# Kernel tuning notes

Hardware: AMD Instinct MI355X
Metric: run time of the kernel (lower is better)

Reference implementation:

```python
import jax, jax.numpy as jnp
import numpy as np

MARGIN = 0.3  # init kwarg, mode='norm'


def _pairwise_dist(X):
    # squared euclidean distances, then safe sqrt (matches euc_dist(X.t()).sqrt())
    sq = jnp.sum(X * X, axis=1)                      # [n]
    d2 = sq[:, None] + sq[None, :] - 2.0 * (X @ X.T)  # [n, n]
    d2 = jnp.maximum(d2, 0.0)
    # safe sqrt: avoid inf derivative at 0 (diagonal); forward value identical
    return jnp.where(d2 > 0.0, jnp.sqrt(jnp.where(d2 > 0.0, d2, 1.0)), 0.0)


def setup_inputs() -> dict:
    key = jax.random.key(0)
    kx, ky = jax.random.split(key)
    X = jax.random.normal(kx, (4096, 2048), dtype=jnp.float32)
    Y = jax.random.randint(ky, (4096,), 0, 128, dtype=jnp.int64)
    return {"X": X, "Y": Y}


def reference(X, Y):
    dist = _pairwise_dist(X)                         # [n, n]
    mask = Y[:, None] == Y[None, :]                  # same-identity mask [n, n]
    inf = jnp.array(jnp.inf, dtype=dist.dtype)
    # hardest positive per anchor: max over same-label entries
    dist_ap = jnp.max(jnp.where(mask, dist, -inf), axis=1)  # [n]
    # hardest negative per anchor: min over different-label entries
    dist_an = jnp.min(jnp.where(mask, inf, dist), axis=1)   # [n]
    # mode == 'norm': mean hinge
    return jnp.mean(jnp.maximum(dist_ap - dist_an + MARGIN, 0.0))
```

## Files before the change

kernel.cpp:

```cpp
#include <hip/hip_runtime.h>
#include <hip/hip_bf16.h>
#include <hip/hip_fp8.h>

typedef __attribute__((ext_vector_type(4))) int i32x4;
typedef __attribute__((ext_vector_type(8))) int i32x8;
typedef __attribute__((ext_vector_type(16))) float f32x16;

#define MARGIN 0.3f
#define BIGF 3.0e38f

__device__ __forceinline__ f32x16 mx_mfma(i32x8 a, i32x8 b, f32x16 c) {
    return __builtin_amdgcn_mfma_scale_f32_32x32x64_f8f6f4(
        a, b, c, 0 , 0 ,
        0, 127 , 0, 127 );
}

__device__ __forceinline__ i32x8 ld32(const unsigned char* p) {
    i32x4 lo = *(const i32x4*)p;
    i32x4 hi = *(const i32x4*)(p + 16);
    return __builtin_shufflevector(lo, hi, 0, 1, 2, 3, 4, 5, 6, 7);
}

__global__ __launch_bounds__(256) void convert_norm_kernel(
    const float* __restrict__ X, unsigned char* __restrict__ Xf,
    float* __restrict__ nrm, unsigned* __restrict__ ap,
    unsigned* __restrict__ an, unsigned* __restrict__ cnt, int K) {
    const int wave = threadIdx.x >> 6, lane = threadIdx.x & 63;
    const int row = blockIdx.x * 4 + wave;
    const float* xr = X + (size_t)row * K;
    const size_t pbase = ((size_t)(row >> 5)) << 16;
    const int rsub = row & 31;
    float s = 0.0f;
    for (int c = lane * 8; c < K; c += 64 * 8) {
        float4 v0 = *(const float4*)(xr + c);
        float4 v1 = *(const float4*)(xr + c + 4);
        float f[8] = {v0.x, v0.y, v0.z, v0.w, v1.x, v1.y, v1.z, v1.w};
        union { unsigned char b[8]; uint2 u; } p;
#pragma unroll
        for (int i = 0; i < 8; i++) {
            __hip_fp8_e4m3 q(f[i]);
            p.b[i] = q.__x;
            float d = (float)q;
            s += d * d;
        }
        const int lslot = rsub + (((c >> 5) & 1) << 5);
        unsigned char* dst = Xf + pbase + ((size_t)(c >> 6) << 11)
                             + (lslot << 5) + (c & 31);
        *(uint2*)dst = p.u;
    }
    for (int off = 32; off > 0; off >>= 1) s += __shfl_xor(s, off, 64);
    if (lane == 0) {
        nrm[row] = s;
        ap[row] = 0u;
        an[row] = 0x7F800000u;
        if (row == 0) *cnt = 0u;
    }
}

__global__ __launch_bounds__(256, 4) void gemm_reduce_kernel(
    const unsigned char* __restrict__ Xf, const float* __restrict__ nrm,
    const int* __restrict__ Y, unsigned* __restrict__ ap,
    unsigned* __restrict__ an, unsigned* __restrict__ cnt,
    float* __restrict__ out, int N, int K) {
    __shared__ int sYr[128], sYc[128];
    __shared__ float sNr[128], sNc[128];
    __shared__ float redmax[4][64], redmin[4][64];
    __shared__ float cmax[4][64], cmin[4][64];
    __shared__ float lsum[4];
    __shared__ unsigned s_done;

    const int tid = threadIdx.x;
    const int wave = tid >> 6;
    const int lane = tid & 63;
    const int m = lane & 31;
    const int h = lane >> 5;
    const int wr = wave >> 1;
    const int wc = wave & 1;

    const int NB = N >> 7;
    const int ntri = NB * (NB + 1) / 2;
    const int FULLB = ntri - 16;
    const int nt = K >> 6;

    if ((int)blockIdx.x < FULLB) {
        int bi = blockIdx.x, ti = 0;
        while (bi >= NB - ti) { bi -= NB - ti; ti++; }
        const int tj = ti + bi;
        const int rowBase = ti << 7;
        const int colBase = tj << 7;

        if (tid < 128) {
            sYr[tid] = Y[rowBase + tid];
            sNr[tid] = nrm[rowBase + tid];
        } else {
            const int t0 = tid - 128;
            sYc[t0] = Y[colBase + t0];
            sNc[t0] = nrm[colBase + t0];
        }

        f32x16 acc[2][2];
#pragma unroll
        for (int si = 0; si < 2; si++)
#pragma unroll
            for (int sj = 0; sj < 2; sj++)
#pragma unroll
                for (int rr = 0; rr < 16; rr++) acc[si][sj][rr] = 0.0f;

        const unsigned char* pa[2];
        const unsigned char* pb[2];
#pragma unroll
        for (int si = 0; si < 2; si++)
            pa[si] = Xf + (((size_t)(rowBase >> 5) + wr * 2 + si) << 16) + lane * 32;
#pragma unroll
        for (int sj = 0; sj < 2; sj++)
            pb[sj] = Xf + (((size_t)(colBase >> 5) + wc * 2 + sj) << 16) + lane * 32;

#pragma unroll 4
        for (int t = 0; t < nt; t++) {
            const size_t off = (size_t)t << 11;
            i32x8 a0 = ld32(pa[0] + off);
            i32x8 a1 = ld32(pa[1] + off);
            i32x8 b0 = ld32(pb[0] + off);
            i32x8 b1 = ld32(pb[1] + off);
            acc[0][0] = mx_mfma(a0, b0, acc[0][0]);
            acc[0][1] = mx_mfma(a0, b1, acc[0][1]);
            acc[1][0] = mx_mfma(a1, b0, acc[1][0]);
            acc[1][1] = mx_mfma(a1, b1, acc[1][1]);
        }

        __syncthreads();

        float cdp[2] = {-1.0f, -1.0f};
        float cdn[2] = {BIGF, BIGF};
#pragma unroll
        for (int si = 0; si < 2; si++)
#pragma unroll
            for (int reg = 0; reg < 16; reg++) {
                const int row64 = si * 32 + (reg & 3) + 8 * (reg >> 2) + 4 * h;
                const int rIdx = wr * 64 + row64;
                const int yr = sYr[rIdx];
                const float nr = sNr[rIdx];
                float dp = -1.0f, dn = BIGF;
#pragma unroll
                for (int sj = 0; sj < 2; sj++) {
                    const int cIdx = wc * 64 + sj * 32 + m;
                    float d2 = nr + sNc[cIdx] - 2.0f * acc[si][sj][reg];
                    float d = sqrtf(fmaxf(d2, 0.0f));
                    bool same = (yr == sYc[cIdx]);
                    float vp = same ? d : -1.0f;
                    float vn = same ? BIGF : d;
                    dp = fmaxf(dp, vp);
                    dn = fminf(dn, vn);
                    cdp[sj] = fmaxf(cdp[sj], vp);
                    cdn[sj] = fminf(cdn[sj], vn);
                }
                for (int off = 1; off < 32; off <<= 1) {
                    dp = fmaxf(dp, __shfl_xor(dp, off, 64));
                    dn = fminf(dn, __shfl_xor(dn, off, 64));
                }
                if (m == 0) {
                    redmax[wave][row64] = dp;
                    redmin[wave][row64] = dn;
                }
            }
#pragma unroll
        for (int sj = 0; sj < 2; sj++) {
            cdp[sj] = fmaxf(cdp[sj], __shfl_xor(cdp[sj], 32, 64));
            cdn[sj] = fminf(cdn[sj], __shfl_xor(cdn[sj], 32, 64));
            if (h == 0) {
                cmax[wave][sj * 32 + m] = cdp[sj];
                cmin[wave][sj * 32 + m] = cdn[sj];
            }
        }
        __syncthreads();

        if (tid < 128) {
            const int wr2 = tid >> 6, r64 = tid & 63;
            float mx = fmaxf(redmax[wr2 * 2][r64], redmax[wr2 * 2 + 1][r64]);
            float mn = fminf(redmin[wr2 * 2][r64], redmin[wr2 * 2 + 1][r64]);
            atomicMax(&ap[rowBase + tid], __float_as_uint(fmaxf(mx, 0.0f)));
            atomicMin(&an[rowBase + tid], __float_as_uint(mn));
        } else {
            const int t0 = tid - 128;
            const int wc2 = t0 >> 6, c64 = t0 & 63;
            float mx = fmaxf(cmax[wc2][c64], cmax[2 + wc2][c64]);
            float mn = fminf(cmin[wc2][c64], cmin[2 + wc2][c64]);
            atomicMax(&ap[colBase + t0], __float_as_uint(fmaxf(mx, 0.0f)));
            atomicMin(&an[colBase + t0], __float_as_uint(mn));
        }
    } else {
        const int qid = blockIdx.x - FULLB;
        int bi = FULLB + (qid >> 2), ti = 0;
        while (bi >= NB - ti) { bi -= NB - ti; ti++; }
        const int tj = ti + bi;
        const int q = qid & 3;
        const int rowBase = (ti << 7) + ((q >> 1) << 6);
        const int colBase = (tj << 7) + ((q & 1) << 6);

        f32x16 acc;
#pragma unroll
        for (int rr = 0; rr < 16; rr++) acc[rr] = 0.0f;

        const unsigned char* pa =
            Xf + (((size_t)(rowBase >> 5) + wr) << 16) + lane * 32;
        const unsigned char* pb =
            Xf + (((size_t)(colBase >> 5) + wc) << 16) + lane * 32;

#pragma unroll 4
        for (int t = 0; t < nt; t++) {
            const size_t off = (size_t)t << 11;
            i32x8 a = ld32(pa + off);
            i32x8 b = ld32(pb + off);
            acc = mx_mfma(a, b, acc);
        }

        const int gc = colBase + wc * 32 + m;
        const int yc = Y[gc];
        const float nc = nrm[gc];
        float cdp = -1.0f, cdn = BIGF;
#pragma unroll
        for (int reg = 0; reg < 16; reg++) {
            const int row32 = (reg & 3) + 8 * (reg >> 2) + 4 * h;
            const int gr = rowBase + wr * 32 + row32;
            const int yr = Y[gr];
            const float nr = nrm[gr];
            float d2 = nr + nc - 2.0f * acc[reg];
            float d = sqrtf(fmaxf(d2, 0.0f));
            bool same = (yr == yc);
            float vp = same ? d : -1.0f;
            float vn = same ? BIGF : d;
            cdp = fmaxf(cdp, vp);
            cdn = fminf(cdn, vn);
            float dp = vp, dn = vn;
            for (int off = 1; off < 32; off <<= 1) {
                dp = fmaxf(dp, __shfl_xor(dp, off, 64));
                dn = fminf(dn, __shfl_xor(dn, off, 64));
            }
            if (m == 0) {
                atomicMax(&ap[gr], __float_as_uint(fmaxf(dp, 0.0f)));
                atomicMin(&an[gr], __float_as_uint(dn));
            }
        }
        cdp = fmaxf(cdp, __shfl_xor(cdp, 32, 64));
        cdn = fminf(cdn, __shfl_xor(cdn, 32, 64));
        if (h == 0) {
            atomicMax(&ap[gc], __float_as_uint(fmaxf(cdp, 0.0f)));
            atomicMin(&an[gc], __float_as_uint(cdn));
        }
    }

    __syncthreads();
    if (tid == 0) {
        __threadfence();
        s_done = atomicAdd(cnt, 1u);
    }
    __syncthreads();
    if (s_done == gridDim.x - 1) {
        __threadfence();
        float s = 0.0f;
        for (int i = tid; i < N; i += 256) {
            unsigned ua = __hip_atomic_load(&ap[i], __ATOMIC_RELAXED,
                                            __HIP_MEMORY_SCOPE_AGENT);
            unsigned ub = __hip_atomic_load(&an[i], __ATOMIC_RELAXED,
                                            __HIP_MEMORY_SCOPE_AGENT);
            s += fmaxf(__uint_as_float(ua) - __uint_as_float(ub) + MARGIN, 0.0f);
        }
        for (int off = 32; off > 0; off >>= 1) s += __shfl_xor(s, off, 64);
        if (lane == 0) lsum[wave] = s;
        __syncthreads();
        if (tid == 0)
            out[0] = (lsum[0] + lsum[1] + lsum[2] + lsum[3]) / (float)N;
    }
}

extern "C" void kernel_launch(void* const* d_in, const int* in_sizes, int n_in,
                              void* d_out, int out_size, void* d_ws, size_t ws_size,
                              hipStream_t stream) {
    const float* X = (const float*)d_in[0];
    const int* Y = (const int*)d_in[1];
    float* out = (float*)d_out;
    const int N = in_sizes[1];
    const int K = in_sizes[0] / N;

    char* ws = (char*)d_ws;
    unsigned char* Xf = (unsigned char*)ws;
    float* nrm = (float*)(ws + (size_t)N * K);
    unsigned* ap = (unsigned*)((char*)nrm + (size_t)N * 4);
    unsigned* an = (unsigned*)((char*)ap + (size_t)N * 4);
    unsigned* cnt = (unsigned*)((char*)an + (size_t)N * 4);

    convert_norm_kernel<<<N / 4, 256, 0, stream>>>(X, Xf, nrm, ap, an, cnt, K);
    const int NB = N / 128;
    const int ntri = NB * (NB + 1) / 2;
    const int grid = (ntri - 16) + 64;
    gemm_reduce_kernel<<<grid, 256, 0, stream>>>(Xf, nrm, Y, ap, an, cnt,
                                                 out, N, K);
}
```

Before: 132.2 us.

## Fuse fp8 conversion into GEMM kernel with per-panel ready flags

Merges the fp32-to-fp8 conversion and norm pass into the GEMM-reduce kernel. The first N/32 blocks each convert a 32-row panel and publish a release flag, and GEMM tiles spin-wait on the flags of the panels they need. This removes one kernel launch and the boundary between the two stages so conversion can overlap GEMM work. In exchange it adds a memset launch, spin-wait cost, and lowers occupancy to 3 blocks per CU. It also relies on the producer blocks being scheduled before or alongside the waiting blocks to avoid deadlock.

```diff
diff --git a/kernel.cpp b/kernel.cpp
--- a/kernel.cpp
+++ b/kernel.cpp
@@ -21,46 +21,18 @@
     return __builtin_shufflevector(lo, hi, 0, 1, 2, 3, 4, 5, 6, 7);
 }
 
-__global__ __launch_bounds__(256) void convert_norm_kernel(
+__device__ __forceinline__ void waitpan(const unsigned* f, int n) {
+    for (int i = 0; i < n; i++)
+        while (__hip_atomic_load(&f[i], __ATOMIC_RELAXED,
+                                 __HIP_MEMORY_SCOPE_AGENT) == 0u)
+            __builtin_amdgcn_s_sleep(2);
+}
+
+__global__ __launch_bounds__(256, 3) void fused_kernel(
     const float* __restrict__ X, unsigned char* __restrict__ Xf,
-    float* __restrict__ nrm, unsigned* __restrict__ ap,
-    unsigned* __restrict__ an, unsigned* __restrict__ cnt, int K) {
-    const int wave = threadIdx.x >> 6, lane = threadIdx.x & 63;
-    const int row = blockIdx.x * 4 + wave;
-    const float* xr = X + (size_t)row * K;
-    const size_t pbase = ((size_t)(row >> 5)) << 16;
-    const int rsub = row & 31;
-    float s = 0.0f;
-    for (int c = lane * 8; c < K; c += 64 * 8) {
-        float4 v0 = *(const float4*)(xr + c);
-        float4 v1 = *(const float4*)(xr + c + 4);
-        float f[8] = {v0.x, v0.y, v0.z, v0.w, v1.x, v1.y, v1.z, v1.w};
-        union { unsigned char b[8]; uint2 u; } p;
-#pragma unroll
-        for (int i = 0; i < 8; i++) {
-            __hip_fp8_e4m3 q(f[i]);
-            p.b[i] = q.__x;
-            float d = (float)q;
-            s += d * d;
-        }
-        const int lslot = rsub + (((c >> 5) & 1) << 5);
-        unsigned char* dst = Xf + pbase + ((size_t)(c >> 6) << 11)
-                             + (lslot << 5) + (c & 31);
-        *(uint2*)dst = p.u;
-    }
-    for (int off = 32; off > 0; off >>= 1) s += __shfl_xor(s, off, 64);
-    if (lane == 0) {
-        nrm[row] = s;
-        ap[row] = 0u;
-        an[row] = 0x7F800000u;
-        if (row == 0) *cnt = 0u;
-    }
-}
-
-__global__ __launch_bounds__(256, 4) void gemm_reduce_kernel(
-    const unsigned char* __restrict__ Xf, const float* __restrict__ nrm,
-    const int* __restrict__ Y, unsigned* __restrict__ ap,
-    unsigned* __restrict__ an, unsigned* __restrict__ cnt,
+    float* __restrict__ nrm, const int* __restrict__ Y,
+    unsigned* __restrict__ ap, unsigned* __restrict__ an,
+    unsigned* __restrict__ flags, unsigned* __restrict__ cnt,
     float* __restrict__ out, int N, int K) {
     __shared__ int sYr[128], sYc[128];
     __shared__ float sNr[128], sNc[128];
@@ -76,18 +48,67 @@
     const int h = lane >> 5;
     const int wr = wave >> 1;
     const int wc = wave & 1;
-
+    const int bid = blockIdx.x;
+
+    const int NPAN = N >> 5;
     const int NB = N >> 7;
     const int ntri = NB * (NB + 1) / 2;
     const int FULLB = ntri - 16;
     const int nt = K >> 6;
 
-    if ((int)blockIdx.x < FULLB) {
-        int bi = blockIdx.x, ti = 0;
+    if (bid < NPAN) {
+#pragma unroll 1
+        for (int r = wave; r < 32; r += 4) {
+            const int row = (bid << 5) + r;
+            const float* xr = X + (size_t)row * K;
+            const size_t pbase = ((size_t)(row >> 5)) << 16;
+            const int rsub = row & 31;
+            float s = 0.0f;
+            for (int c = lane * 8; c < K; c += 64 * 8) {
+                float4 v0 = *(const float4*)(xr + c);
+                float4 v1 = *(const float4*)(xr + c + 4);
+                float f[8] = {v0.x, v0.y, v0.z, v0.w, v1.x, v1.y, v1.z, v1.w};
+                union { unsigned char b[8]; uint2 u; } p;
+#pragma unroll
+                for (int i = 0; i < 8; i++) {
+                    __hip_fp8_e4m3 q(f[i]);
+                    p.b[i] = q.__x;
+                    float d = (float)q;
+                    s += d * d;
+                }
+                const int lslot = rsub + (((c >> 5) & 1) << 5);
+                unsigned char* dst = Xf + pbase + ((size_t)(c >> 6) << 11)
+                                     + (lslot << 5) + (c & 31);
+                *(uint2*)dst = p.u;
+            }
+            for (int off = 32; off > 0; off >>= 1) s += __shfl_xor(s, off, 64);
+            if (lane == 0) {
+                nrm[row] = s;
+                ap[row] = 0u;
+                an[row] = 0x7F800000u;
+            }
+        }
+        __syncthreads();
+        if (tid == 0) {
+            __threadfence();
+            __hip_atomic_store(&flags[bid], 1u, __ATOMIC_RELEASE,
+                               __HIP_MEMORY_SCOPE_AGENT);
+        }
+    }
+
+    if (bid < FULLB) {
+        int bi = bid, ti = 0;
         while (bi >= NB - ti) { bi -= NB - ti; ti++; }
         const int tj = ti + bi;
         const int rowBase = ti << 7;
         const int colBase = tj << 7;
+
+        if (tid == 0) {
+            waitpan(flags + (rowBase >> 5), 4);
+            waitpan(flags + (colBase >> 5), 4);
+            __threadfence();
+        }
+        __syncthreads();
 
         if (tid < 128) {
             sYr[tid] = Y[rowBase + tid];
@@ -189,13 +210,20 @@
             atomicMin(&an[colBase + t0], __float_as_uint(mn));
         }
     } else {
-        const int qid = blockIdx.x - FULLB;
+        const int qid = bid - FULLB;
         int bi = FULLB + (qid >> 2), ti = 0;
         while (bi >= NB - ti) { bi -= NB - ti; ti++; }
         const int tj = ti + bi;
         const int q = qid & 3;
         const int rowBase = (ti << 7) + ((q >> 1) << 6);
         const int colBase = (tj << 7) + ((q & 1) << 6);
+
+        if (tid == 0) {
+            waitpan(flags + (rowBase >> 5), 2);
+            waitpan(flags + (colBase >> 5), 2);
+            __threadfence();
+        }
+        __syncthreads();
 
         f32x16 acc;
 #pragma unroll
@@ -285,14 +313,16 @@
     char* ws = (char*)d_ws;
     unsigned char* Xf = (unsigned char*)ws;
     float* nrm = (float*)(ws + (size_t)N * K);
-    unsigned* ap = (unsigned*)((char*)nrm + (size_t)N * 4);
-    unsigned* an = (unsigned*)((char*)ap + (size_t)N * 4);
-    unsigned* cnt = (unsigned*)((char*)an + (size_t)N * 4);
-
-    convert_norm_kernel<<<N / 4, 256, 0, stream>>>(X, Xf, nrm, ap, an, cnt, K);
+    unsigned* ap = (unsigned*)(nrm + N);
+    unsigned* an = ap + N;
+    unsigned* flags = an + N;
+    unsigned* cnt = flags + (N >> 5);
+
+    hipMemsetAsync(flags, 0, ((N >> 5) + 1) * sizeof(unsigned), stream);
+
     const int NB = N / 128;
     const int ntri = NB * (NB + 1) / 2;
     const int grid = (ntri - 16) + 64;
-    gemm_reduce_kernel<<<grid, 256, 0, stream>>>(Xf, nrm, Y, ap, an, cnt,
-                                                 out, N, K);
-}
+    fused_kernel<<<grid, 256, 0, stream>>>(X, Xf, nrm, Y, ap, an, flags,
+                                           cnt, out, N, K);
+}
```

After: 153.8 us. +16.3%, slower.
